# Kernel tuning notes

Measured on AMD Instinct MI355X. Metric: run time of the kernel, lower is better.

The kernel has to match this reference:

```python
import jax, jax.numpy as jnp
import numpy as np

B, T, H = 16384, 64, 8
VOCABS = [2, 2, 21, 22, 5, 2, 22, 24]
EDIMS = [1, 1, 3, 3, 1, 1, 3, 3]


def _lstm_layer(xs, W_ih, W_hh, b_ih, b_hh):
    # xs: [B, T, F] -> hidden sequence [B, T, H]; torch gate order (i, f, g, o)
    Bsz = xs.shape[0]
    Hd = W_hh.shape[1]

    def step(carry, x_t):
        h, c = carry
        gates = x_t @ W_ih.T + b_ih + h @ W_hh.T + b_hh  # [B, 4H]
        i, f, g, o = jnp.split(gates, 4, axis=-1)
        c = jax.nn.sigmoid(f) * c + jax.nn.sigmoid(i) * jnp.tanh(g)
        h = jax.nn.sigmoid(o) * jnp.tanh(c)
        return (h, c), h

    init = (jnp.zeros((Bsz, Hd), xs.dtype), jnp.zeros((Bsz, Hd), xs.dtype))
    _, hs = jax.lax.scan(step, init, jnp.swapaxes(xs, 0, 1))  # scan over time
    return jnp.swapaxes(hs, 0, 1)


def setup_inputs() -> dict:
    key = jax.random.key(0)
    ks = jax.random.split(key, 40)
    cols = [jax.random.randint(ks[i], (B, T, 1), 0, VOCABS[i], dtype=jnp.int32) for i in range(8)]
    x = jnp.concatenate(cols, axis=2)  # [B, T, 8] categorical ids

    def p(k, shape):
        return jax.random.normal(k, shape, jnp.float32) * 0.1

    d = {"x": x}
    for i in range(8):
        d["e" + str(i + 1)] = p(ks[8 + i], (VOCABS[i], EDIMS[i]))
    d["W_ih0"] = p(ks[16], (4 * H, 16)); d["W_hh0"] = p(ks[17], (4 * H, H))
    d["b_ih0"] = p(ks[18], (4 * H,));   d["b_hh0"] = p(ks[19], (4 * H,))
    d["W_ih1"] = p(ks[20], (4 * H, H)); d["W_hh1"] = p(ks[21], (4 * H, H))
    d["b_ih1"] = p(ks[22], (4 * H,));   d["b_hh1"] = p(ks[23], (4 * H,))
    d["fc6_w"] = p(ks[24], (4, H)); d["fc6_b"] = p(ks[25], (4,))
    d["fc7_w"] = p(ks[26], (1, 4)); d["fc7_b"] = p(ks[27], (1,))
    d["fc1_w"] = p(ks[28], (4, H)); d["fc1_b"] = p(ks[29], (4,))
    d["fc2_w"] = p(ks[30], (1, 4)); d["fc2_b"] = p(ks[31], (1,))
    d["fc3_w"] = p(ks[32], (1, T)); d["fc3_b"] = p(ks[33], (1,))
    return d


def reference(x, e1, e2, e3, e4, e5, e6, e7, e8,
              W_ih0, W_hh0, b_ih0, b_hh0, W_ih1, W_hh1, b_ih1, b_hh1,
              fc6_w, fc6_b, fc7_w, fc7_b, fc1_w, fc1_b, fc2_w, fc2_b, fc3_w, fc3_b):
    tabs = (e1, e2, e3, e4, e5, e6, e7, e8)
    # 8-way embedding lookup + concat -> [B, T, 16]
    emb = jnp.concatenate([tabs[i][x[:, :, i]] for i in range(8)], axis=2)
    h1 = _lstm_layer(emb, W_ih0, W_hh0, b_ih0, b_hh0)
    out = _lstm_layer(h1, W_ih1, W_hh1, b_ih1, b_hh1)  # [B, T, H]
    # tiny dual FC branches applied per (b, t) position
    theta = ((out @ fc6_w.T + fc6_b) @ fc7_w.T + fc7_b)[..., 0]  # [B, T]
    h = ((out @ fc1_w.T + fc1_b) @ fc2_w.T + fc2_b)[..., 0]      # [B, T]
    pred = (theta * h) @ fc3_w.T + fc3_b  # [B, 1]
    return pred
```

## Files before the change

### kernel.cpp

```cpp
#include <hip/hip_runtime.h>
#include <hip/hip_bf16.h>

typedef float f2 __attribute__((ext_vector_type(2)));

__device__ __forceinline__ float sigf(float x) {
  return __builtin_amdgcn_rcpf(1.0f + __expf(-x));
}
__device__ __forceinline__ float tanh_fast(float x) {
  return fmaf(-2.0f, __builtin_amdgcn_rcpf(1.0f + __expf(2.0f * x)), 1.0f);
}

__launch_bounds__(256, 2)
__global__ void lstm_fused(
    const int* __restrict__ x,
    const float* __restrict__ e1, const float* __restrict__ e2,
    const float* __restrict__ e3, const float* __restrict__ e4,
    const float* __restrict__ e5, const float* __restrict__ e6,
    const float* __restrict__ e7, const float* __restrict__ e8,
    const float* __restrict__ W_ih0, const float* __restrict__ W_hh0,
    const float* __restrict__ b_ih0, const float* __restrict__ b_hh0,
    const float* __restrict__ W_ih1, const float* __restrict__ W_hh1,
    const float* __restrict__ b_ih1, const float* __restrict__ b_hh1,
    const float* __restrict__ fc6_w, const float* __restrict__ fc6_b,
    const float* __restrict__ fc7_w, const float* __restrict__ fc7_b,
    const float* __restrict__ fc1_w, const float* __restrict__ fc1_b,
    const float* __restrict__ fc2_w, const float* __restrict__ fc2_b,
    const float* __restrict__ fc3_w, const float* __restrict__ fc3_b,
    float* __restrict__ out)
{
  __shared__ __align__(16) float sTf[3200];
  __shared__ float sW3[64];
  __shared__ __align__(16) float sH0[256];
  __shared__ __align__(16) float sH1[256];

  const int tid = threadIdx.x;

  {
    constexpr int RO[8]  = {0,2,4,25,47,52,54,76};
    constexpr int ED[8]  = {1,1,3,3,1,1,3,3};
    constexpr int CO[8]  = {0,1,2,5,8,9,10,13};
    constexpr int VOC[8] = {2,2,21,22,5,2,22,24};
    const float* ep[8] = {e1,e2,e3,e4,e5,e6,e7,e8};
    #pragma unroll
    for (int f = 0; f < 8; ++f) {
      const float* E = ep[f];
      for (int idx = tid; idx < VOC[f]*32; idx += 256) {
        int v = idx >> 5, m = idx & 31;
        int jj = m >> 2, q = m & 3, g = q*8 + jj;
        float s = 0.0f;
        #pragma unroll
        for (int d = 0; d < ED[f]; ++d)
          s += E[v*ED[f]+d] * W_ih0[g*16 + CO[f] + d];
        if (f == 0) s += b_ih0[g] + b_hh0[g];
        sTf[(RO[f]+v)*32 + m] = s;
      }
    }
    if (tid < 64) sW3[tid] = fc3_w[tid];
  }
  __syncthreads();

  const int j = tid & 7;
  const int b = (blockIdx.x << 5) + (tid >> 3);

  f2 wIF0[8], wGO0[8], iIF1[8], iGO1[8], rIF1[8], rGO1[8];
  {
    const float4* P;
    float4 I0,I1,F0,F1,G0,G1,O0,O1;
    #define LOADROWS(M) \
      P = (const float4*)(M); \
      I0 = P[(0*8+j)*2]; I1 = P[(0*8+j)*2+1]; \
      F0 = P[(1*8+j)*2]; F1 = P[(1*8+j)*2+1]; \
      G0 = P[(2*8+j)*2]; G1 = P[(2*8+j)*2+1]; \
      O0 = P[(3*8+j)*2]; O1 = P[(3*8+j)*2+1];
    #define PACK(dIF, dGO) \
      dIF[0]=(f2){I0.x,F0.x}; dIF[1]=(f2){I0.y,F0.y}; dIF[2]=(f2){I0.z,F0.z}; dIF[3]=(f2){I0.w,F0.w}; \
      dIF[4]=(f2){I1.x,F1.x}; dIF[5]=(f2){I1.y,F1.y}; dIF[6]=(f2){I1.z,F1.z}; dIF[7]=(f2){I1.w,F1.w}; \
      dGO[0]=(f2){G0.x,O0.x}; dGO[1]=(f2){G0.y,O0.y}; dGO[2]=(f2){G0.z,O0.z}; dGO[3]=(f2){G0.w,O0.w}; \
      dGO[4]=(f2){G1.x,O1.x}; dGO[5]=(f2){G1.y,O1.y}; dGO[6]=(f2){G1.z,O1.z}; dGO[7]=(f2){G1.w,O1.w};
    LOADROWS(W_hh0); PACK(wIF0, wGO0);
    LOADROWS(W_ih1); PACK(iIF1, iGO1);
    LOADROWS(W_hh1); PACK(rIF1, rGO1);
    #undef LOADROWS
    #undef PACK
  }
  const f2 bIF1 = {b_ih1[j]    + b_hh1[j],    b_ih1[8+j]  + b_hh1[8+j]};
  const f2 bGO1 = {b_ih1[16+j] + b_hh1[16+j], b_ih1[24+j] + b_hh1[24+j]};

  f2 uvk[8];
  float f7[4], f2c[4];
  #pragma unroll
  for (int q = 0; q < 4; ++q) { f7[q] = fc7_w[q]; f2c[q] = fc2_w[q]; }
  #pragma unroll
  for (int k = 0; k < 8; ++k) {
    float s1 = 0.f, s2 = 0.f;
    #pragma unroll
    for (int q = 0; q < 4; ++q) {
      s1 += f7[q]  * fc6_w[q*8+k];
      s2 += f2c[q] * fc1_w[q*8+k];
    }
    uvk[k] = (f2){s1, s2};
  }
  float cth = fc7_b[0], chh = fc2_b[0];
  #pragma unroll
  for (int q = 0; q < 4; ++q) { cth += f7[q]*fc6_b[q]; chh += f2c[q]*fc1_b[q]; }
  const f2 cc = {cth, chh};
  const float fc3b = fc3_b[0];

  float h0s[8];
  #pragma unroll
  for (int k = 0; k < 8; ++k) h0s[k] = 0.f;
  float c0 = 0.f, c1 = 0.f, acc = 0.f;

  sH1[tid] = 0.f;

  const int4* xp = (const int4*)(x + (size_t)b * 512);
  int4 ia = xp[0], ib = xp[1];
  const float4* tf4 = (const float4*)sTf;
  const float4* ph0 = (const float4*)&sH0[tid & ~7];
  const float4* ph1 = (const float4*)&sH1[tid & ~7];

  #pragma unroll 1
  for (int t = 0; t < 64; ++t) {
    float4 h1A = ph1[0], h1B = ph1[1];
    float h1s[8] = {h1A.x,h1A.y,h1A.z,h1A.w,h1B.x,h1B.y,h1B.z,h1B.w};

    const int tn = (t < 63) ? (2*t + 2) : 126;
    int4 na = xp[tn], nb = xp[tn+1];
    const float w3p = (t == 0) ? 0.f : sW3[t-1];

    float4 g0 = tf4[(      ia.x)*8 + j];
    float4 g1 = tf4[(  2 + ia.y)*8 + j];
    float4 g2 = tf4[(  4 + ia.z)*8 + j];
    float4 g3 = tf4[( 25 + ia.w)*8 + j];
    float4 g4 = tf4[( 47 + ib.x)*8 + j];
    float4 g5 = tf4[( 52 + ib.y)*8 + j];
    float4 g6 = tf4[( 54 + ib.z)*8 + j];
    float4 g7 = tf4[( 76 + ib.w)*8 + j];
    f2 gIF = (((f2){g0.x,g0.y} + (f2){g1.x,g1.y}) + ((f2){g2.x,g2.y} + (f2){g3.x,g3.y}))
           + (((f2){g4.x,g4.y} + (f2){g5.x,g5.y}) + ((f2){g6.x,g6.y} + (f2){g7.x,g7.y}));
    f2 gGO = (((f2){g0.z,g0.w} + (f2){g1.z,g1.w}) + ((f2){g2.z,g2.w} + (f2){g3.z,g3.w}))
           + (((f2){g4.z,g4.w} + (f2){g5.z,g5.w}) + ((f2){g6.z,g6.w} + (f2){g7.z,g7.w}));

    #pragma unroll
    for (int k = 0; k < 8; ++k) {
      f2 hb = (f2)(h0s[k]);
      gIF = __builtin_elementwise_fma(wIF0[k], hb, gIF);
      gGO = __builtin_elementwise_fma(wGO0[k], hb, gGO);
    }
    float si = sigf(gIF.x), sf = sigf(gIF.y), tg = tanh_fast(gGO.x), so = sigf(gGO.y);
    c0 = fmaf(sf, c0, si * tg);
    float h0 = so * tanh_fast(c0);
    sH0[tid] = h0;

    f2 GIF = bIF1, GGO = bGO1, thf = cc;
    #pragma unroll
    for (int k = 0; k < 8; ++k) {
      f2 hb = (f2)(h1s[k]);
      GIF = __builtin_elementwise_fma(rIF1[k], hb, GIF);
      GGO = __builtin_elementwise_fma(rGO1[k], hb, GGO);
      thf = __builtin_elementwise_fma(uvk[k],  hb, thf);
    }
    acc = fmaf(thf.x * thf.y, w3p, acc);

    {
      float4 lo = ph0[0], hi = ph0[1];
      h0s[0]=lo.x; h0s[1]=lo.y; h0s[2]=lo.z; h0s[3]=lo.w;
      h0s[4]=hi.x; h0s[5]=hi.y; h0s[6]=hi.z; h0s[7]=hi.w;
    }

    #pragma unroll
    for (int k = 0; k < 8; ++k) {
      f2 hb = (f2)(h0s[k]);
      GIF = __builtin_elementwise_fma(iIF1[k], hb, GIF);
      GGO = __builtin_elementwise_fma(iGO1[k], hb, GGO);
    }
    float si1 = sigf(GIF.x), sf1 = sigf(GIF.y), tg1 = tanh_fast(GGO.x), so1 = sigf(GGO.y);
    c1 = fmaf(sf1, c1, si1 * tg1);
    float h1 = so1 * tanh_fast(c1);
    sH1[tid] = h1;

    ia = na; ib = nb;
  }

  {
    float4 h1A = ph1[0], h1B = ph1[1];
    float h1s[8] = {h1A.x,h1A.y,h1A.z,h1A.w,h1B.x,h1B.y,h1B.z,h1B.w};
    f2 thf = cc;
    #pragma unroll
    for (int k = 0; k < 8; ++k)
      thf = __builtin_elementwise_fma(uvk[k], (f2)(h1s[k]), thf);
    acc = fmaf(thf.x * thf.y, sW3[63], acc);
  }

  if (j == 0) out[b] = acc + fc3b;
}

extern "C" void kernel_launch(void* const* d_in, const int* in_sizes, int n_in,
                              void* d_out, int out_size, void* d_ws, size_t ws_size,
                              hipStream_t stream) {
  const int* x = (const int*)d_in[0];
  const float *E1=(const float*)d_in[1],  *E2=(const float*)d_in[2],
              *E3=(const float*)d_in[3],  *E4=(const float*)d_in[4],
              *E5=(const float*)d_in[5],  *E6=(const float*)d_in[6],
              *E7=(const float*)d_in[7],  *E8=(const float*)d_in[8];
  const float *Wih0=(const float*)d_in[9],  *Whh0=(const float*)d_in[10],
              *bih0=(const float*)d_in[11], *bhh0=(const float*)d_in[12],
              *Wih1=(const float*)d_in[13], *Whh1=(const float*)d_in[14],
              *bih1=(const float*)d_in[15], *bhh1=(const float*)d_in[16],
              *fc6w=(const float*)d_in[17], *fc6b=(const float*)d_in[18],
              *fc7w=(const float*)d_in[19], *fc7b=(const float*)d_in[20],
              *fc1w=(const float*)d_in[21], *fc1b=(const float*)d_in[22],
              *fc2w=(const float*)d_in[23], *fc2b=(const float*)d_in[24],
              *fc3w=(const float*)d_in[25], *fc3b=(const float*)d_in[26];

  lstm_fused<<<512, 256, 0, stream>>>(
      x, E1,E2,E3,E4,E5,E6,E7,E8,
      Wih0, Whh0, bih0, bhh0, Wih1, Whh1, bih1, bhh1,
      fc6w, fc6b, fc7w, fc7b, fc1w, fc1b, fc2w, fc2b, fc3w, fc3b,
      (float*)d_out);
}
```

Baseline: 167.8 us.

## Exchange LSTM hidden states via DPP lane shuffles instead of shared memory

Hidden states h0 and h1 are now broadcast across the 8 lanes of each batch row with DPP permutes (quad_perm and row_mirror patterns), using XOR-permuted weight registers, in place of writes and reads through shared-memory arrays. This takes LDS traffic and its latency out of the serial recurrence. The embedding-table gathers are also software-pipelined one step ahead, the FMA chains are split into two accumulators to shorten dependency chains, and the fc3 weights are shifted so the t==0 branch disappears. It adds extra registers for the prefetched gathers and split accumulators, and depends on the DPP lane mapping being correct.

```diff
diff --git a/kernel.cpp b/kernel.cpp
--- a/kernel.cpp
+++ b/kernel.cpp
@@ -8,6 +8,24 @@
 }
 __device__ __forceinline__ float tanh_fast(float x) {
   return fmaf(-2.0f, __builtin_amdgcn_rcpf(1.0f + __expf(2.0f * x)), 1.0f);
+}
+
+template<int CTRL>
+__device__ __forceinline__ float dppf(float v) {
+  return __builtin_bit_cast(float,
+      __builtin_amdgcn_mov_dpp(__builtin_bit_cast(int, v), CTRL, 0xf, 0xf, false));
+}
+
+__device__ __forceinline__ void fanout8(float h, float* d) {
+  d[0] = h;
+  d[1] = dppf<0xB1>(h);
+  d[2] = dppf<0x4E>(h);
+  d[3] = dppf<0x1B>(h);
+  float t7 = dppf<0x141>(h);
+  d[7] = t7;
+  d[4] = dppf<0x1B>(t7);
+  d[5] = dppf<0x4E>(t7);
+  d[6] = dppf<0xB1>(t7);
 }
 
 __launch_bounds__(256, 2)
@@ -29,9 +47,7 @@
     float* __restrict__ out)
 {
   __shared__ __align__(16) float sTf[3200];
-  __shared__ float sW3[64];
-  __shared__ __align__(16) float sH0[256];
-  __shared__ __align__(16) float sH1[256];
+  __shared__ float sW3s[65];
 
   const int tid = threadIdx.x;
 
@@ -55,7 +71,8 @@
         sTf[(RO[f]+v)*32 + m] = s;
       }
     }
-    if (tid < 64) sW3[tid] = fc3_w[tid];
+    if (tid < 64) sW3s[tid+1] = fc3_w[tid];
+    if (tid == 64) sW3s[0] = 0.f;
   }
   __syncthreads();
 
@@ -63,42 +80,33 @@
   const int b = (blockIdx.x << 5) + (tid >> 3);
 
   f2 wIF0[8], wGO0[8], iIF1[8], iGO1[8], rIF1[8], rGO1[8];
-  {
-    const float4* P;
-    float4 I0,I1,F0,F1,G0,G1,O0,O1;
-    #define LOADROWS(M) \
-      P = (const float4*)(M); \
-      I0 = P[(0*8+j)*2]; I1 = P[(0*8+j)*2+1]; \
-      F0 = P[(1*8+j)*2]; F1 = P[(1*8+j)*2+1]; \
-      G0 = P[(2*8+j)*2]; G1 = P[(2*8+j)*2+1]; \
-      O0 = P[(3*8+j)*2]; O1 = P[(3*8+j)*2+1];
-    #define PACK(dIF, dGO) \
-      dIF[0]=(f2){I0.x,F0.x}; dIF[1]=(f2){I0.y,F0.y}; dIF[2]=(f2){I0.z,F0.z}; dIF[3]=(f2){I0.w,F0.w}; \
-      dIF[4]=(f2){I1.x,F1.x}; dIF[5]=(f2){I1.y,F1.y}; dIF[6]=(f2){I1.z,F1.z}; dIF[7]=(f2){I1.w,F1.w}; \
-      dGO[0]=(f2){G0.x,O0.x}; dGO[1]=(f2){G0.y,O0.y}; dGO[2]=(f2){G0.z,O0.z}; dGO[3]=(f2){G0.w,O0.w}; \
-      dGO[4]=(f2){G1.x,O1.x}; dGO[5]=(f2){G1.y,O1.y}; dGO[6]=(f2){G1.z,O1.z}; dGO[7]=(f2){G1.w,O1.w};
-    LOADROWS(W_hh0); PACK(wIF0, wGO0);
-    LOADROWS(W_ih1); PACK(iIF1, iGO1);
-    LOADROWS(W_hh1); PACK(rIF1, rGO1);
-    #undef LOADROWS
-    #undef PACK
+  #pragma unroll
+  for (int r = 0; r < 8; ++r) {
+    const int k = j ^ r;
+    wIF0[r] = (f2){W_hh0[(0*8+j)*8+k], W_hh0[(1*8+j)*8+k]};
+    wGO0[r] = (f2){W_hh0[(2*8+j)*8+k], W_hh0[(3*8+j)*8+k]};
+    iIF1[r] = (f2){W_ih1[(0*8+j)*8+k], W_ih1[(1*8+j)*8+k]};
+    iGO1[r] = (f2){W_ih1[(2*8+j)*8+k], W_ih1[(3*8+j)*8+k]};
+    rIF1[r] = (f2){W_hh1[(0*8+j)*8+k], W_hh1[(1*8+j)*8+k]};
+    rGO1[r] = (f2){W_hh1[(2*8+j)*8+k], W_hh1[(3*8+j)*8+k]};
   }
   const f2 bIF1 = {b_ih1[j]    + b_hh1[j],    b_ih1[8+j]  + b_hh1[8+j]};
   const f2 bGO1 = {b_ih1[16+j] + b_hh1[16+j], b_ih1[24+j] + b_hh1[24+j]};
 
+  float f7[4], f2c[4];
+  #pragma unroll
+  for (int q = 0; q < 4; ++q) { f7[q] = fc7_w[q]; f2c[q] = fc2_w[q]; }
   f2 uvk[8];
-  float f7[4], f2c[4];
-  #pragma unroll
-  for (int q = 0; q < 4; ++q) { f7[q] = fc7_w[q]; f2c[q] = fc2_w[q]; }
-  #pragma unroll
-  for (int k = 0; k < 8; ++k) {
+  #pragma unroll
+  for (int r = 0; r < 8; ++r) {
+    const int k = j ^ r;
     float s1 = 0.f, s2 = 0.f;
     #pragma unroll
     for (int q = 0; q < 4; ++q) {
       s1 += f7[q]  * fc6_w[q*8+k];
       s2 += f2c[q] * fc1_w[q*8+k];
     }
-    uvk[k] = (f2){s1, s2};
+    uvk[r] = (f2){s1, s2};
   }
   float cth = fc7_b[0], chh = fc2_b[0];
   #pragma unroll
@@ -106,90 +114,101 @@
   const f2 cc = {cth, chh};
   const float fc3b = fc3_b[0];
 
-  float h0s[8];
-  #pragma unroll
-  for (int k = 0; k < 8; ++k) h0s[k] = 0.f;
+  float h0x[8], h1x[8];
+  #pragma unroll
+  for (int k = 0; k < 8; ++k) { h0x[k] = 0.f; h1x[k] = 0.f; }
   float c0 = 0.f, c1 = 0.f, acc = 0.f;
 
-  sH1[tid] = 0.f;
-
   const int4* xp = (const int4*)(x + (size_t)b * 512);
+  const float4* tf4 = (const float4*)sTf;
+
   int4 ia = xp[0], ib = xp[1];
-  const float4* tf4 = (const float4*)sTf;
-  const float4* ph0 = (const float4*)&sH0[tid & ~7];
-  const float4* ph1 = (const float4*)&sH1[tid & ~7];
+  float4 G0 = tf4[(      ia.x)*8 + j];
+  float4 G1 = tf4[(  2 + ia.y)*8 + j];
+  float4 G2 = tf4[(  4 + ia.z)*8 + j];
+  float4 G3 = tf4[( 25 + ia.w)*8 + j];
+  float4 G4 = tf4[( 47 + ib.x)*8 + j];
+  float4 G5 = tf4[( 52 + ib.y)*8 + j];
+  float4 G6 = tf4[( 54 + ib.z)*8 + j];
+  float4 G7 = tf4[( 76 + ib.w)*8 + j];
+  int4 na = xp[2], nb = xp[3];
 
   #pragma unroll 1
   for (int t = 0; t < 64; ++t) {
-    float4 h1A = ph1[0], h1B = ph1[1];
-    float h1s[8] = {h1A.x,h1A.y,h1A.z,h1A.w,h1B.x,h1B.y,h1B.z,h1B.w};
-
-    const int tn = (t < 63) ? (2*t + 2) : 126;
-    int4 na = xp[tn], nb = xp[tn+1];
-    const float w3p = (t == 0) ? 0.f : sW3[t-1];
-
-    float4 g0 = tf4[(      ia.x)*8 + j];
-    float4 g1 = tf4[(  2 + ia.y)*8 + j];
-    float4 g2 = tf4[(  4 + ia.z)*8 + j];
-    float4 g3 = tf4[( 25 + ia.w)*8 + j];
-    float4 g4 = tf4[( 47 + ib.x)*8 + j];
-    float4 g5 = tf4[( 52 + ib.y)*8 + j];
-    float4 g6 = tf4[( 54 + ib.z)*8 + j];
-    float4 g7 = tf4[( 76 + ib.w)*8 + j];
-    f2 gIF = (((f2){g0.x,g0.y} + (f2){g1.x,g1.y}) + ((f2){g2.x,g2.y} + (f2){g3.x,g3.y}))
-           + (((f2){g4.x,g4.y} + (f2){g5.x,g5.y}) + ((f2){g6.x,g6.y} + (f2){g7.x,g7.y}));
-    f2 gGO = (((f2){g0.z,g0.w} + (f2){g1.z,g1.w}) + ((f2){g2.z,g2.w} + (f2){g3.z,g3.w}))
-           + (((f2){g4.z,g4.w} + (f2){g5.z,g5.w}) + ((f2){g6.z,g6.w} + (f2){g7.z,g7.w}));
-
-    #pragma unroll
-    for (int k = 0; k < 8; ++k) {
-      f2 hb = (f2)(h0s[k]);
-      gIF = __builtin_elementwise_fma(wIF0[k], hb, gIF);
-      gGO = __builtin_elementwise_fma(wGO0[k], hb, gGO);
-    }
+    const float w3p = sW3s[t];
+
+    f2 sIFa = ((f2){G0.x,G0.y} + (f2){G1.x,G1.y}) + ((f2){G2.x,G2.y} + (f2){G3.x,G3.y});
+    f2 sIFb = ((f2){G4.x,G4.y} + (f2){G5.x,G5.y}) + ((f2){G6.x,G6.y} + (f2){G7.x,G7.y});
+    f2 sGOa = ((f2){G0.z,G0.w} + (f2){G1.z,G1.w}) + ((f2){G2.z,G2.w} + (f2){G3.z,G3.w});
+    f2 sGOb = ((f2){G4.z,G4.w} + (f2){G5.z,G5.w}) + ((f2){G6.z,G6.w} + (f2){G7.z,G7.w});
+
+    G0 = tf4[(      na.x)*8 + j];
+    G1 = tf4[(  2 + na.y)*8 + j];
+    G2 = tf4[(  4 + na.z)*8 + j];
+    G3 = tf4[( 25 + na.w)*8 + j];
+    G4 = tf4[( 47 + nb.x)*8 + j];
+    G5 = tf4[( 52 + nb.y)*8 + j];
+    G6 = tf4[( 54 + nb.z)*8 + j];
+    G7 = tf4[( 76 + nb.w)*8 + j];
+
+    {
+      const int tn = (2*t + 4 <= 126) ? (2*t + 4) : 126;
+      na = xp[tn]; nb = xp[tn+1];
+    }
+
+    f2 GIFa = bIF1, GIFb = (f2){0.f,0.f}, GGOa = bGO1, GGOb = (f2){0.f,0.f};
+    f2 thfa = cc,  thfb = (f2){0.f,0.f};
+    #pragma unroll
+    for (int r = 0; r < 8; r += 2) {
+      f2 hA = (f2)(h1x[r]), hB = (f2)(h1x[r+1]);
+      GIFa = __builtin_elementwise_fma(rIF1[r],   hA, GIFa);
+      GIFb = __builtin_elementwise_fma(rIF1[r+1], hB, GIFb);
+      GGOa = __builtin_elementwise_fma(rGO1[r],   hA, GGOa);
+      GGOb = __builtin_elementwise_fma(rGO1[r+1], hB, GGOb);
+      thfa = __builtin_elementwise_fma(uvk[r],    hA, thfa);
+      thfb = __builtin_elementwise_fma(uvk[r+1],  hB, thfb);
+    }
+    f2 thf = thfa + thfb;
+    acc = fmaf(thf.x * thf.y, w3p, acc);
+
+    #pragma unroll
+    for (int r = 0; r < 8; r += 2) {
+      sIFa = __builtin_elementwise_fma(wIF0[r],   (f2)(h0x[r]),   sIFa);
+      sIFb = __builtin_elementwise_fma(wIF0[r+1], (f2)(h0x[r+1]), sIFb);
+      sGOa = __builtin_elementwise_fma(wGO0[r],   (f2)(h0x[r]),   sGOa);
+      sGOb = __builtin_elementwise_fma(wGO0[r+1], (f2)(h0x[r+1]), sGOb);
+    }
+    f2 gIF = sIFa + sIFb, gGO = sGOa + sGOb;
     float si = sigf(gIF.x), sf = sigf(gIF.y), tg = tanh_fast(gGO.x), so = sigf(gGO.y);
     c0 = fmaf(sf, c0, si * tg);
     float h0 = so * tanh_fast(c0);
-    sH0[tid] = h0;
-
-    f2 GIF = bIF1, GGO = bGO1, thf = cc;
-    #pragma unroll
-    for (int k = 0; k < 8; ++k) {
-      f2 hb = (f2)(h1s[k]);
-      GIF = __builtin_elementwise_fma(rIF1[k], hb, GIF);
-      GGO = __builtin_elementwise_fma(rGO1[k], hb, GGO);
-      thf = __builtin_elementwise_fma(uvk[k],  hb, thf);
-    }
-    acc = fmaf(thf.x * thf.y, w3p, acc);
-
-    {
-      float4 lo = ph0[0], hi = ph0[1];
-      h0s[0]=lo.x; h0s[1]=lo.y; h0s[2]=lo.z; h0s[3]=lo.w;
-      h0s[4]=hi.x; h0s[5]=hi.y; h0s[6]=hi.z; h0s[7]=hi.w;
-    }
-
-    #pragma unroll
-    for (int k = 0; k < 8; ++k) {
-      f2 hb = (f2)(h0s[k]);
-      GIF = __builtin_elementwise_fma(iIF1[k], hb, GIF);
-      GGO = __builtin_elementwise_fma(iGO1[k], hb, GGO);
-    }
+
+    fanout8(h0, h0x);
+
+    #pragma unroll
+    for (int r = 0; r < 8; r += 2) {
+      GIFa = __builtin_elementwise_fma(iIF1[r],   (f2)(h0x[r]),   GIFa);
+      GIFb = __builtin_elementwise_fma(iIF1[r+1], (f2)(h0x[r+1]), GIFb);
+      GGOa = __builtin_elementwise_fma(iGO1[r],   (f2)(h0x[r]),   GGOa);
+      GGOb = __builtin_elementwise_fma(iGO1[r+1], (f2)(h0x[r+1]), GGOb);
+    }
+    f2 GIF = GIFa + GIFb, GGO = GGOa + GGOb;
     float si1 = sigf(GIF.x), sf1 = sigf(GIF.y), tg1 = tanh_fast(GGO.x), so1 = sigf(GGO.y);
     c1 = fmaf(sf1, c1, si1 * tg1);
     float h1 = so1 * tanh_fast(c1);
-    sH1[tid] = h1;
-
-    ia = na; ib = nb;
+
+    fanout8(h1, h1x);
   }
 
   {
-    float4 h1A = ph1[0], h1B = ph1[1];
-    float h1s[8] = {h1A.x,h1A.y,h1A.z,h1A.w,h1B.x,h1B.y,h1B.z,h1B.w};
-    f2 thf = cc;
-    #pragma unroll
-    for (int k = 0; k < 8; ++k)
-      thf = __builtin_elementwise_fma(uvk[k], (f2)(h1s[k]), thf);
-    acc = fmaf(thf.x * thf.y, sW3[63], acc);
+    f2 thfa = cc, thfb = (f2){0.f,0.f};
+    #pragma unroll
+    for (int r = 0; r < 8; r += 2) {
+      thfa = __builtin_elementwise_fma(uvk[r],   (f2)(h1x[r]),   thfa);
+      thfb = __builtin_elementwise_fma(uvk[r+1], (f2)(h1x[r+1]), thfb);
+    }
+    f2 thf = thfa + thfb;
+    acc = fmaf(thf.x * thf.y, sW3s[64], acc);
   }
 
   if (j == 0) out[b] = acc + fc3b;
```

Result: slower. 179.7 us (+7.0%).

## Process two batch rows per thread group to interleave independent LSTM chains

Applied to the files above, without the earlier changes.

Each 8-thread group now handles two sequences (A and B) at once, so two independent recurrence dependency chains are interleaved to hide latency from transcendental ops and LDS round-trips. The grid is halved to 256 blocks and launch bounds relaxed to one block per CU, giving more registers per thread. Embedding-table gathers are software-pipelined one step ahead, and layer-0 FMAs are split into two partial accumulators. The cost is higher register pressure and half as many blocks, which may leave some CUs idle on a 256-CU device.

```diff
diff --git a/kernel.cpp b/kernel.cpp
--- a/kernel.cpp
+++ b/kernel.cpp
@@ -10,7 +10,7 @@
   return fmaf(-2.0f, __builtin_amdgcn_rcpf(1.0f + __expf(2.0f * x)), 1.0f);
 }
 
-__launch_bounds__(256, 2)
+__launch_bounds__(256, 1)
 __global__ void lstm_fused(
     const int* __restrict__ x,
     const float* __restrict__ e1, const float* __restrict__ e2,
@@ -29,9 +29,9 @@
     float* __restrict__ out)
 {
   __shared__ __align__(16) float sTf[3200];
-  __shared__ float sW3[64];
-  __shared__ __align__(16) float sH0[256];
-  __shared__ __align__(16) float sH1[256];
+  __shared__ float sW3s[65];
+  __shared__ __align__(16) float sH0[512];
+  __shared__ __align__(16) float sH1[512];
 
   const int tid = threadIdx.x;
 
@@ -55,28 +55,31 @@
         sTf[(RO[f]+v)*32 + m] = s;
       }
     }
-    if (tid < 64) sW3[tid] = fc3_w[tid];
+    if (tid < 64) sW3s[tid+1] = fc3_w[tid];
+    if (tid == 64) sW3s[0] = 0.f;
   }
   __syncthreads();
 
   const int j = tid & 7;
-  const int b = (blockIdx.x << 5) + (tid >> 3);
+  const int bA = (blockIdx.x << 6) + ((tid >> 3) << 1);
+
+  sH1[tid] = 0.f;  sH1[256 + tid] = 0.f;
 
   f2 wIF0[8], wGO0[8], iIF1[8], iGO1[8], rIF1[8], rGO1[8];
   {
     const float4* P;
-    float4 I0,I1,F0,F1,G0,G1,O0,O1;
+    float4 I0,I1,F0,F1,G0_,G1_,O0,O1;
     #define LOADROWS(M) \
       P = (const float4*)(M); \
       I0 = P[(0*8+j)*2]; I1 = P[(0*8+j)*2+1]; \
       F0 = P[(1*8+j)*2]; F1 = P[(1*8+j)*2+1]; \
-      G0 = P[(2*8+j)*2]; G1 = P[(2*8+j)*2+1]; \
+      G0_ = P[(2*8+j)*2]; G1_ = P[(2*8+j)*2+1]; \
       O0 = P[(3*8+j)*2]; O1 = P[(3*8+j)*2+1];
     #define PACK(dIF, dGO) \
       dIF[0]=(f2){I0.x,F0.x}; dIF[1]=(f2){I0.y,F0.y}; dIF[2]=(f2){I0.z,F0.z}; dIF[3]=(f2){I0.w,F0.w}; \
       dIF[4]=(f2){I1.x,F1.x}; dIF[5]=(f2){I1.y,F1.y}; dIF[6]=(f2){I1.z,F1.z}; dIF[7]=(f2){I1.w,F1.w}; \
-      dGO[0]=(f2){G0.x,O0.x}; dGO[1]=(f2){G0.y,O0.y}; dGO[2]=(f2){G0.z,O0.z}; dGO[3]=(f2){G0.w,O0.w}; \
-      dGO[4]=(f2){G1.x,O1.x}; dGO[5]=(f2){G1.y,O1.y}; dGO[6]=(f2){G1.z,O1.z}; dGO[7]=(f2){G1.w,O1.w};
+      dGO[0]=(f2){G0_.x,O0.x}; dGO[1]=(f2){G0_.y,O0.y}; dGO[2]=(f2){G0_.z,O0.z}; dGO[3]=(f2){G0_.w,O0.w}; \
+      dGO[4]=(f2){G1_.x,O1.x}; dGO[5]=(f2){G1_.y,O1.y}; dGO[6]=(f2){G1_.z,O1.z}; dGO[7]=(f2){G1_.w,O1.w};
     LOADROWS(W_hh0); PACK(wIF0, wGO0);
     LOADROWS(W_ih1); PACK(iIF1, iGO1);
     LOADROWS(W_hh1); PACK(rIF1, rGO1);
@@ -106,93 +109,149 @@
   const f2 cc = {cth, chh};
   const float fc3b = fc3_b[0];
 
-  float h0s[8];
-  #pragma unroll
-  for (int k = 0; k < 8; ++k) h0s[k] = 0.f;
-  float c0 = 0.f, c1 = 0.f, acc = 0.f;
-
-  sH1[tid] = 0.f;
-
-  const int4* xp = (const int4*)(x + (size_t)b * 512);
-  int4 ia = xp[0], ib = xp[1];
+  float h0sA[8], h0sB[8];
+  #pragma unroll
+  for (int k = 0; k < 8; ++k) { h0sA[k] = 0.f; h0sB[k] = 0.f; }
+  float c0A = 0.f, c1A = 0.f, accA = 0.f;
+  float c0B = 0.f, c1B = 0.f, accB = 0.f;
+
+  const int4* xpA = (const int4*)(x + (size_t)bA * 512);
+  const int4* xpB = xpA + 128;
   const float4* tf4 = (const float4*)sTf;
-  const float4* ph0 = (const float4*)&sH0[tid & ~7];
-  const float4* ph1 = (const float4*)&sH1[tid & ~7];
+  const float4* phA0 = (const float4*)&sH0[tid & ~7];
+  const float4* phB0 = (const float4*)&sH0[256 + (tid & ~7)];
+  const float4* phA1 = (const float4*)&sH1[tid & ~7];
+  const float4* phB1 = (const float4*)&sH1[256 + (tid & ~7)];
+
+  int4 iaA = xpA[0], ibA = xpA[1], iaB = xpB[0], ibB = xpB[1];
+  float4 GA0 = tf4[(      iaA.x)*8 + j], GB0 = tf4[(      iaB.x)*8 + j];
+  float4 GA1 = tf4[(  2 + iaA.y)*8 + j], GB1 = tf4[(  2 + iaB.y)*8 + j];
+  float4 GA2 = tf4[(  4 + iaA.z)*8 + j], GB2 = tf4[(  4 + iaB.z)*8 + j];
+  float4 GA3 = tf4[( 25 + iaA.w)*8 + j], GB3 = tf4[( 25 + iaB.w)*8 + j];
+  float4 GA4 = tf4[( 47 + ibA.x)*8 + j], GB4 = tf4[( 47 + ibB.x)*8 + j];
+  float4 GA5 = tf4[( 52 + ibA.y)*8 + j], GB5 = tf4[( 52 + ibB.y)*8 + j];
+  float4 GA6 = tf4[( 54 + ibA.z)*8 + j], GB6 = tf4[( 54 + ibB.z)*8 + j];
+  float4 GA7 = tf4[( 76 + ibA.w)*8 + j], GB7 = tf4[( 76 + ibB.w)*8 + j];
+  int4 naA = xpA[2], nbA = xpA[3], naB = xpB[2], nbB = xpB[3];
 
   #pragma unroll 1
   for (int t = 0; t < 64; ++t) {
-    float4 h1A = ph1[0], h1B = ph1[1];
-    float h1s[8] = {h1A.x,h1A.y,h1A.z,h1A.w,h1B.x,h1B.y,h1B.z,h1B.w};
-
-    const int tn = (t < 63) ? (2*t + 2) : 126;
-    int4 na = xp[tn], nb = xp[tn+1];
-    const float w3p = (t == 0) ? 0.f : sW3[t-1];
-
-    float4 g0 = tf4[(      ia.x)*8 + j];
-    float4 g1 = tf4[(  2 + ia.y)*8 + j];
-    float4 g2 = tf4[(  4 + ia.z)*8 + j];
-    float4 g3 = tf4[( 25 + ia.w)*8 + j];
-    float4 g4 = tf4[( 47 + ib.x)*8 + j];
-    float4 g5 = tf4[( 52 + ib.y)*8 + j];
-    float4 g6 = tf4[( 54 + ib.z)*8 + j];
-    float4 g7 = tf4[( 76 + ib.w)*8 + j];
-    f2 gIF = (((f2){g0.x,g0.y} + (f2){g1.x,g1.y}) + ((f2){g2.x,g2.y} + (f2){g3.x,g3.y}))
-           + (((f2){g4.x,g4.y} + (f2){g5.x,g5.y}) + ((f2){g6.x,g6.y} + (f2){g7.x,g7.y}));
-    f2 gGO = (((f2){g0.z,g0.w} + (f2){g1.z,g1.w}) + ((f2){g2.z,g2.w} + (f2){g3.z,g3.w}))
-           + (((f2){g4.z,g4.w} + (f2){g5.z,g5.w}) + ((f2){g6.z,g6.w} + (f2){g7.z,g7.w}));
-
+    const float w3p = sW3s[t];
+
+    float4 hA1a = phA1[0], hA1b = phA1[1];
+    float4 hB1a = phB1[0], hB1b = phB1[1];
+    float h1sA[8] = {hA1a.x,hA1a.y,hA1a.z,hA1a.w,hA1b.x,hA1b.y,hA1b.z,hA1b.w};
+    float h1sB[8] = {hB1a.x,hB1a.y,hB1a.z,hB1a.w,hB1b.x,hB1b.y,hB1b.z,hB1b.w};
+
+    f2 sIFAa = ((f2){GA0.x,GA0.y} + (f2){GA1.x,GA1.y}) + ((f2){GA2.x,GA2.y} + (f2){GA3.x,GA3.y});
+    f2 sIFAb = ((f2){GA4.x,GA4.y} + (f2){GA5.x,GA5.y}) + ((f2){GA6.x,GA6.y} + (f2){GA7.x,GA7.y});
+    f2 sGOAa = ((f2){GA0.z,GA0.w} + (f2){GA1.z,GA1.w}) + ((f2){GA2.z,GA2.w} + (f2){GA3.z,GA3.w});
+    f2 sGOAb = ((f2){GA4.z,GA4.w} + (f2){GA5.z,GA5.w}) + ((f2){GA6.z,GA6.w} + (f2){GA7.z,GA7.w});
+    f2 sIFBa = ((f2){GB0.x,GB0.y} + (f2){GB1.x,GB1.y}) + ((f2){GB2.x,GB2.y} + (f2){GB3.x,GB3.y});
+    f2 sIFBb = ((f2){GB4.x,GB4.y} + (f2){GB5.x,GB5.y}) + ((f2){GB6.x,GB6.y} + (f2){GB7.x,GB7.y});
+    f2 sGOBa = ((f2){GB0.z,GB0.w} + (f2){GB1.z,GB1.w}) + ((f2){GB2.z,GB2.w} + (f2){GB3.z,GB3.w});
+    f2 sGOBb = ((f2){GB4.z,GB4.w} + (f2){GB5.z,GB5.w}) + ((f2){GB6.z,GB6.w} + (f2){GB7.z,GB7.w});
+
+    GA0 = tf4[(      naA.x)*8 + j];  GB0 = tf4[(      naB.x)*8 + j];
+    GA1 = tf4[(  2 + naA.y)*8 + j];  GB1 = tf4[(  2 + naB.y)*8 + j];
+    GA2 = tf4[(  4 + naA.z)*8 + j];  GB2 = tf4[(  4 + naB.z)*8 + j];
+    GA3 = tf4[( 25 + naA.w)*8 + j];  GB3 = tf4[( 25 + naB.w)*8 + j];
+    GA4 = tf4[( 47 + nbA.x)*8 + j];  GB4 = tf4[( 47 + nbB.x)*8 + j];
+    GA5 = tf4[( 52 + nbA.y)*8 + j];  GB5 = tf4[( 52 + nbB.y)*8 + j];
+    GA6 = tf4[( 54 + nbA.z)*8 + j];  GB6 = tf4[( 54 + nbB.z)*8 + j];
+    GA7 = tf4[( 76 + nbA.w)*8 + j];  GB7 = tf4[( 76 + nbB.w)*8 + j];
+
+    {
+      const int tn = (2*t + 4 <= 126) ? (2*t + 4) : 126;
+      naA = xpA[tn]; nbA = xpA[tn+1];
+      naB = xpB[tn]; nbB = xpB[tn+1];
+    }
+
+    f2 GIFA = bIF1, GGOA = bGO1, thfA = cc;
+    f2 GIFB = bIF1, GGOB = bGO1, thfB = cc;
     #pragma unroll
     for (int k = 0; k < 8; ++k) {
-      f2 hb = (f2)(h0s[k]);
-      gIF = __builtin_elementwise_fma(wIF0[k], hb, gIF);
-      gGO = __builtin_elementwise_fma(wGO0[k], hb, gGO);
-    }
-    float si = sigf(gIF.x), sf = sigf(gIF.y), tg = tanh_fast(gGO.x), so = sigf(gGO.y);
-    c0 = fmaf(sf, c0, si * tg);
-    float h0 = so * tanh_fast(c0);
-    sH0[tid] = h0;
-
-    f2 GIF = bIF1, GGO = bGO1, thf = cc;
+      f2 hA = (f2)(h1sA[k]), hB = (f2)(h1sB[k]);
+      GIFA = __builtin_elementwise_fma(rIF1[k], hA, GIFA);
+      GGOA = __builtin_elementwise_fma(rGO1[k], hA, GGOA);
+      thfA = __builtin_elementwise_fma(uvk[k],  hA, thfA);
+      GIFB = __builtin_elementwise_fma(rIF1[k], hB, GIFB);
+      GGOB = __builtin_elementwise_fma(rGO1[k], hB, GGOB);
+      thfB = __builtin_elementwise_fma(uvk[k],  hB, thfB);
+    }
+    accA = fmaf(thfA.x * thfA.y, w3p, accA);
+    accB = fmaf(thfB.x * thfB.y, w3p, accB);
+
+    #pragma unroll
+    for (int k = 0; k < 8; k += 2) {
+      sIFAa = __builtin_elementwise_fma(wIF0[k],   (f2)(h0sA[k]),   sIFAa);
+      sIFAb = __builtin_elementwise_fma(wIF0[k+1], (f2)(h0sA[k+1]), sIFAb);
+      sGOAa = __builtin_elementwise_fma(wGO0[k],   (f2)(h0sA[k]),   sGOAa);
+      sGOAb = __builtin_elementwise_fma(wGO0[k+1], (f2)(h0sA[k+1]), sGOAb);
+      sIFBa = __builtin_elementwise_fma(wIF0[k],   (f2)(h0sB[k]),   sIFBa);
+      sIFBb = __builtin_elementwise_fma(wIF0[k+1], (f2)(h0sB[k+1]), sIFBb);
+      sGOBa = __builtin_elementwise_fma(wGO0[k],   (f2)(h0sB[k]),   sGOBa);
+      sGOBb = __builtin_elementwise_fma(wGO0[k+1], (f2)(h0sB[k+1]), sGOBb);
+    }
+    f2 gIFA = sIFAa + sIFAb, gGOA = sGOAa + sGOAb;
+    f2 gIFB = sIFBa + sIFBb, gGOB = sGOBa + sGOBb;
+    float siA = sigf(gIFA.x), sfA = sigf(gIFA.y), tgA = tanh_fast(gGOA.x), soA = sigf(gGOA.y);
+    float siB = sigf(gIFB.x), sfB = sigf(gIFB.y), tgB = tanh_fast(gGOB.x), soB = sigf(gGOB.y);
+    c0A = fmaf(sfA, c0A, siA * tgA);
+    c0B = fmaf(sfB, c0B, siB * tgB);
+    float h0A = soA * tanh_fast(c0A);
+    float h0B = soB * tanh_fast(c0B);
+    sH0[tid] = h0A;
+    sH0[256 + tid] = h0B;
+
+    {
+      float4 lo = phA0[0], hi = phA0[1];
+      h0sA[0]=lo.x; h0sA[1]=lo.y; h0sA[2]=lo.z; h0sA[3]=lo.w;
+      h0sA[4]=hi.x; h0sA[5]=hi.y; h0sA[6]=hi.z; h0sA[7]=hi.w;
+    }
+    {
+      float4 lo = phB0[0], hi = phB0[1];
+      h0sB[0]=lo.x; h0sB[1]=lo.y; h0sB[2]=lo.z; h0sB[3]=lo.w;
+      h0sB[4]=hi.x; h0sB[5]=hi.y; h0sB[6]=hi.z; h0sB[7]=hi.w;
+    }
+
     #pragma unroll
     for (int k = 0; k < 8; ++k) {
-      f2 hb = (f2)(h1s[k]);
-      GIF = __builtin_elementwise_fma(rIF1[k], hb, GIF);
-      GGO = __builtin_elementwise_fma(rGO1[k], hb, GGO);
-      thf = __builtin_elementwise_fma(uvk[k],  hb, thf);
-    }
-    acc = fmaf(thf.x * thf.y, w3p, acc);
-
-    {
-      float4 lo = ph0[0], hi = ph0[1];
-      h0s[0]=lo.x; h0s[1]=lo.y; h0s[2]=lo.z; h0s[3]=lo.w;
-      h0s[4]=hi.x; h0s[5]=hi.y; h0s[6]=hi.z; h0s[7]=hi.w;
-    }
-
+      f2 hA = (f2)(h0sA[k]), hB = (f2)(h0sB[k]);
+      GIFA = __builtin_elementwise_fma(iIF1[k], hA, GIFA);
+      GGOA = __builtin_elementwise_fma(iGO1[k], hA, GGOA);
+      GIFB = __builtin_elementwise_fma(iIF1[k], hB, GIFB);
+      GGOB = __builtin_elementwise_fma(iGO1[k], hB, GGOB);
+    }
+    float si1A = sigf(GIFA.x), sf1A = sigf(GIFA.y), tg1A = tanh_fast(GGOA.x), so1A = sigf(GGOA.y);
+    float si1B = sigf(GIFB.x), sf1B = sigf(GIFB.y), tg1B = tanh_fast(GGOB.x), so1B = sigf(GGOB.y);
+    c1A = fmaf(sf1A, c1A, si1A * tg1A);
+    c1B = fmaf(sf1B, c1B, si1B * tg1B);
+    float h1A = so1A * tanh_fast(c1A);
+    float h1B = so1B * tanh_fast(c1B);
+    sH1[tid] = h1A;
+    sH1[256 + tid] = h1B;
+  }
+
+  {
+    float4 hA1a = phA1[0], hA1b = phA1[1];
+    float4 hB1a = phB1[0], hB1b = phB1[1];
+    float h1sA[8] = {hA1a.x,hA1a.y,hA1a.z,hA1a.w,hA1b.x,hA1b.y,hA1b.z,hA1b.w};
+    float h1sB[8] = {hB1a.x,hB1a.y,hB1a.z,hB1a.w,hB1b.x,hB1b.y,hB1b.z,hB1b.w};
+    f2 thfA = cc, thfB = cc;
     #pragma unroll
     for (int k = 0; k < 8; ++k) {
-      f2 hb = (f2)(h0s[k]);
-      GIF = __builtin_elementwise_fma(iIF1[k], hb, GIF);
-      GGO = __builtin_elementwise_fma(iGO1[k], hb, GGO);
-    }
-    float si1 = sigf(GIF.x), sf1 = sigf(GIF.y), tg1 = tanh_fast(GGO.x), so1 = sigf(GGO.y);
-    c1 = fmaf(sf1, c1, si1 * tg1);
-    float h1 = so1 * tanh_fast(c1);
-    sH1[tid] = h1;
-
-    ia = na; ib = nb;
-  }
-
-  {
-    float4 h1A = ph1[0], h1B = ph1[1];
-    float h1s[8] = {h1A.x,h1A.y,h1A.z,h1A.w,h1B.x,h1B.y,h1B.z,h1B.w};
-    f2 thf = cc;
-    #pragma unroll
-    for (int k = 0; k < 8; ++k)
-      thf = __builtin_elementwise_fma(uvk[k], (f2)(h1s[k]), thf);
-    acc = fmaf(thf.x * thf.y, sW3[63], acc);
-  }
-
-  if (j == 0) out[b] = acc + fc3b;
+      thfA = __builtin_elementwise_fma(uvk[k], (f2)(h1sA[k]), thfA);
+      thfB = __builtin_elementwise_fma(uvk[k], (f2)(h1sB[k]), thfB);
+    }
+    accA = fmaf(thfA.x * thfA.y, sW3s[64], accA);
+    accB = fmaf(thfB.x * thfB.y, sW3s[64], accB);
+  }
+
+  if (j == 0) {
+    out[bA]     = accA + fc3b;
+    out[bA + 1] = accB + fc3b;
+  }
 }
 
 extern "C" void kernel_launch(void* const* d_in, const int* in_sizes, int n_in,
@@ -213,7 +272,7 @@
               *fc2w=(const float*)d_in[23], *fc2b=(const float*)d_in[24],
               *fc3w=(const float*)d_in[25], *fc3b=(const float*)d_in[26];
 
-  lstm_fused<<<512, 256, 0, stream>>>(
+  lstm_fused<<<256, 256, 0, stream>>>(
       x, E1,E2,E3,E4,E5,E6,E7,E8,
       Wih0, Whh0, bih0, bhh0, Wih1, Whh1, bih1, bhh1,
       fc6w, fc6b, fc7w, fc7b, fc1w, fc1b, fc2w, fc2b, fc3w, fc3b,
```

Measured after the change: 177.9 us. +6.0%, slower.
